# Optimization experiments

Hardware: AMD Instinct MI355X
Metric: run time of the kernel (lower is better)

The kernel has to match this reference:

```python
import jax, jax.numpy as jnp
import numpy as np

BS, IN_F, OUT_F = 1024, 128, 100000
M, S, ALPHA = 0.35, 30.0, 0.5


def _l2norm(x):
    # F.normalize: x / max(||x||, eps)
    n = jnp.sqrt(jnp.sum(x * x, axis=-1, keepdims=True))
    return x / jnp.maximum(n, 1e-12)


def setup_inputs() -> dict:
    key = jax.random.key(0)
    k1, k2, k3 = jax.random.split(key, 3)
    return {
        "input": jax.random.normal(k1, (BS, IN_F), dtype=jnp.float32),
        "label": jax.random.randint(k2, (BS,), 0, OUT_F, dtype=jnp.int64),
        "weight": jax.random.normal(k3, (OUT_F, IN_F), dtype=jnp.float32),
    }


def reference(input, label, weight):
    wn = _l2norm(weight)                      # [nc, d]
    fn = _l2norm(input)                       # [bs, d]
    logits = jnp.einsum('bd,cd->bc', fn, wn)  # [bs, nc] cosine sims
    bs = fn.shape[0]
    rows = jnp.arange(bs)

    pos = jnp.take_along_axis(logits, label[:, None], axis=1)[:, 0] * S  # [bs]
    # negatives: all classes except the label (replaces masked_select + view)
    neg = (logits * S).at[rows, label].set(-jnp.inf)
    lse_neg = jax.nn.logsumexp(neg, axis=1)   # [bs]

    # loss = mean(log(1 + exp(m + lse_neg - pos)))
    loss = jnp.mean(jax.nn.softplus(M + lse_neg - pos))

    # weight.data update: per-class mean of normalized features for classes
    # present in the batch (the torch loop is exactly a segment-mean; note
    # weight_update aliases weight.data so the final blend is a no-op and the
    # result is simply: present rows <- class mean, other rows unchanged).
    sums = jax.ops.segment_sum(fn, label, num_segments=OUT_F)                # [nc, d]
    counts = jax.ops.segment_sum(jnp.ones((bs,), fn.dtype), label, num_segments=OUT_F)
    present = counts > 0
    class_mean = sums / jnp.maximum(counts, 1.0)[:, None]
    new_weight = jnp.where(present[:, None], class_mean, weight)

    return loss, new_weight
```

## Files before the change

kernel.cpp:

```cpp
#include <hip/hip_runtime.h>

#define BS 1024
#define D 128
#define NC 100000
#define NCP 100096
#define NTILES 782
#define S_SCALE 30.0f
#define MARGIN 0.35f
#define GRIDX 64

typedef __attribute__((ext_vector_type(8))) short bf16x8;
typedef __attribute__((ext_vector_type(4))) float f32x4;

__device__ __forceinline__ unsigned short f2bf(float f) {
    union { float f; unsigned u; } x; x.f = f;
    unsigned u = x.u;
    u += 0x7FFFu + ((u >> 16) & 1u);
    return (unsigned short)(u >> 16);
}

__device__ __forceinline__ void gld_lds16(const void* g, void* l) {
    auto gp = (const __attribute__((address_space(1))) unsigned int*)(g);
    auto lp = (__attribute__((address_space(3))) unsigned int*)(l);
    __builtin_amdgcn_global_load_lds(gp, lp, 16, 0, 0);
}

__global__ void prep_fn(const float* __restrict__ inp, const int* __restrict__ label,
                        const float* __restrict__ wt,
                        float* __restrict__ fn_f32, unsigned short* __restrict__ fn_sw,
                        float* __restrict__ counts, float* __restrict__ pos) {
    int row = blockIdx.x;
    int lane = threadIdx.x;
    float2 v = *(const float2*)(inp + row * D + lane * 2);
    float s = v.x * v.x + v.y * v.y;
    #pragma unroll
    for (int m = 1; m < 64; m <<= 1) s += __shfl_xor(s, m);
    float inv = 1.0f / fmaxf(sqrtf(s), 1e-12f);
    float a = v.x * inv, b = v.y * inv;
    *(float2*)(fn_f32 + row * D + lane * 2) = make_float2(a, b);
    unsigned pack = (unsigned)f2bf(a) | ((unsigned)f2bf(b) << 16);
    ((unsigned*)fn_sw)[row * 64 + (((lane >> 2) ^ (row & 15)) << 2) + (lane & 3)] = pack;

    int c = label[row];
    float2 wv = *(const float2*)(wt + c * D + lane * 2);
    float sw_ = wv.x * wv.x + wv.y * wv.y;
    float dt  = wv.x * a + wv.y * b;
    #pragma unroll
    for (int m = 1; m < 64; m <<= 1) { sw_ += __shfl_xor(sw_, m); dt += __shfl_xor(dt, m); }
    if (lane == 0) {
        float invw = 1.0f / fmaxf(sqrtf(sw_), 1e-12f);
        pos[row] = S_SCALE * dt * invw;
        atomicAdd(counts + c, 1.0f);
    }
}

__global__ void prep_wn(const float* __restrict__ wt, const float* __restrict__ counts,
                        unsigned short* __restrict__ wn_sw, float* __restrict__ outw) {
    int wv = threadIdx.x >> 6, lane = threadIdx.x & 63;
    int row = blockIdx.x * 4 + wv;
    int t = row >> 7, c = row & 127;
    unsigned* dst = (unsigned*)wn_sw + t * 8192 + c * 64 +
                    (((lane >> 2) ^ (c & 15)) << 2) + (lane & 3);
    if (row < NC) {
        float2 v = *(const float2*)(wt + row * D + lane * 2);
        float s = v.x * v.x + v.y * v.y;
        #pragma unroll
        for (int m = 1; m < 64; m <<= 1) s += __shfl_xor(s, m);
        float inv = 1.0f / fmaxf(sqrtf(s), 1e-12f);
        *dst = (unsigned)f2bf(v.x * inv) | ((unsigned)f2bf(v.y * inv) << 16);
        float cnt = counts[row];
        float2 o = (cnt > 0.0f) ? make_float2(0.0f, 0.0f) : v;
        *(float2*)(outw + row * D + lane * 2) = o;
    } else {
        *dst = 0u;
    }
}

__global__ __launch_bounds__(256, 2) void main_gemm(
    const unsigned short* __restrict__ fnsw, const unsigned short* __restrict__ wnsw,
    float* __restrict__ sumexp) {
    __shared__ __align__(16) short As[128 * 128];
    __shared__ __align__(16) short Bs[128 * 128];
    int tid = threadIdx.x;
    int lane = tid & 63, w = tid >> 6;
    int quad = lane >> 4, l15 = lane & 15;
    int m0 = (w >> 1) * 64, n0 = (w & 1) * 64;
    int rowbase = blockIdx.y * 128;

    {
        const char* gA = (const char*)fnsw + rowbase * 256 + w * 8192 + lane * 16;
        char* lA = (char*)As + w * 8192;
        #pragma unroll
        for (int j = 0; j < 8; j++) gld_lds16(gA + j * 1024, lA + j * 1024);
    }

    float sums[16];
    #pragma unroll
    for (int i = 0; i < 16; i++) sums[i] = 0.0f;

    for (int tile = blockIdx.x; tile < NTILES; tile += GRIDX) {
        const char* gB = (const char*)wnsw + tile * 32768 + w * 8192 + lane * 16;
        char* lB = (char*)Bs + w * 8192;
        __syncthreads();
        #pragma unroll
        for (int j = 0; j < 8; j++) gld_lds16(gB + j * 1024, lB + j * 1024);
        __syncthreads();

        f32x4 acc[4][4];
        #pragma unroll
        for (int mt = 0; mt < 4; mt++)
            #pragma unroll
            for (int nt = 0; nt < 4; nt++)
                acc[mt][nt] = (f32x4){0.0f, 0.0f, 0.0f, 0.0f};

        #pragma unroll
        for (int ks = 0; ks < 4; ks++) {
            int kb = ks * 4 + quad;
            bf16x8 af[4], bf[4];
            #pragma unroll
            for (int mt = 0; mt < 4; mt++) {
                int row = m0 + mt * 16 + l15;
                af[mt] = *(const bf16x8*)(As + (row * 16 + (kb ^ l15)) * 8);
            }
            #pragma unroll
            for (int nt = 0; nt < 4; nt++) {
                int row = n0 + nt * 16 + l15;
                bf[nt] = *(const bf16x8*)(Bs + (row * 16 + (kb ^ l15)) * 8);
            }
            #pragma unroll
            for (int mt = 0; mt < 4; mt++)
                #pragma unroll
                for (int nt = 0; nt < 4; nt++)
                    acc[mt][nt] = __builtin_amdgcn_mfma_f32_16x16x32_bf16(
                        af[mt], bf[nt], acc[mt][nt], 0, 0, 0);
        }

        #pragma unroll
        for (int nt = 0; nt < 4; nt++)
            #pragma unroll
            for (int mt = 0; mt < 4; mt++)
                #pragma unroll
                for (int r = 0; r < 4; r++)
                    sums[mt * 4 + r] += __expf(fmaf(acc[mt][nt][r], S_SCALE, -30.0f));
    }

    #pragma unroll
    for (int mt = 0; mt < 4; mt++) {
        #pragma unroll
        for (int r = 0; r < 4; r++) {
            float s = sums[mt * 4 + r];
            s += __shfl_xor(s, 1);
            s += __shfl_xor(s, 2);
            s += __shfl_xor(s, 4);
            s += __shfl_xor(s, 8);
            if (l15 == 0)
                atomicAdd(sumexp + rowbase + m0 + mt * 16 + quad * 4 + r, s);
        }
    }
}

__global__ void loss_k(const float* __restrict__ sumexp, const float* __restrict__ pos,
                       float* __restrict__ out) {
    __shared__ float red[256];
    int t = threadIdx.x;
    float acc = 0.0f;
    #pragma unroll
    for (int i = 0; i < 4; i++) {
        int r = t + i * 256;
        float p = pos[r];
        float sneg = fmaxf(sumexp[r] - __expf(p - 30.0f), 1e-38f);
        float lse = 30.0f + logf(sneg);
        float z = MARGIN + lse - p;
        acc += fmaxf(z, 0.0f) + log1pf(__expf(-fabsf(z)));
    }
    red[t] = acc;
    __syncthreads();
    for (int s = 128; s > 0; s >>= 1) {
        if (t < s) red[t] += red[t + s];
        __syncthreads();
    }
    if (t == 0) out[0] = red[0] * (1.0f / 1024.0f);
}

__global__ void addmean_k(const float* __restrict__ fn_f32, const int* __restrict__ label,
                          const float* __restrict__ counts, float* __restrict__ outw) {
    int b = blockIdx.x, t = threadIdx.x;
    int c = label[b];
    float cnt = counts[c];
    atomicAdd(outw + c * D + t, fn_f32[b * D + t] / cnt);
}

extern "C" void kernel_launch(void* const* d_in, const int* in_sizes, int n_in,
                              void* d_out, int out_size, void* d_ws, size_t ws_size,
                              hipStream_t stream) {
    (void)in_sizes; (void)n_in; (void)out_size; (void)ws_size;
    const float* inp   = (const float*)d_in[0];
    const int*   label = (const int*)d_in[1];
    const float* wt    = (const float*)d_in[2];
    float* out = (float*)d_out;

    char* w = (char*)d_ws;
    float*          fn_f32 = (float*)(w);
    unsigned short* fn_sw  = (unsigned short*)(w + 524288);
    unsigned short* wn_sw  = (unsigned short*)(w + 786432);
    float*          sumexp = (float*)(w + 26411008);
    float*          counts = (float*)(w + 26415104);
    float*          pos    = (float*)(w + 26815104);

    hipMemsetAsync(w + 26411008, 0, 404096, stream);

    prep_fn<<<BS, 64, 0, stream>>>(inp, label, wt, fn_f32, fn_sw, counts, pos);
    prep_wn<<<NCP / 4, 256, 0, stream>>>(wt, counts, wn_sw, out + 1);
    main_gemm<<<dim3(GRIDX, 8), 256, 0, stream>>>(fn_sw, wn_sw, sumexp);
    addmean_k<<<BS, D, 0, stream>>>(fn_f32, label, counts, out + 1);
    loss_k<<<1, 256, 0, stream>>>(sumexp, pos, out);
}
```

Measured before the change: 162.7 us.

## Fuse loss and class-mean into prep/GEMM kernels, keep A in registers, use exp2

Several changes land together. The class-mean weight update moves into prep_fn, which accumulates per-slot sums, and prep_wn, which writes the mean directly, so the addmean kernel goes away. The loss reduction moves into the GEMM's last-finishing block through a ticket counter, so loss_k goes away. The GEMM now keeps the A fragments in registers with a single LDS buffer, folds the scale into the features so it can use exp2, and changes grid and occupancy (GRIDX 96, launch bounds 3). These cut launches and LDS traffic, at the cost of more atomics and higher register pressure.

```diff
diff --git a/kernel.cpp b/kernel.cpp
--- a/kernel.cpp
+++ b/kernel.cpp
@@ -7,7 +7,9 @@
 #define NTILES 782
 #define S_SCALE 30.0f
 #define MARGIN 0.35f
-#define GRIDX 64
+#define GRIDX 96
+#define GRID_TOTAL (GRIDX * 8)
+#define C_EXP 43.280851226668917f
 
 typedef __attribute__((ext_vector_type(8))) short bf16x8;
 typedef __attribute__((ext_vector_type(4))) float f32x4;
@@ -19,6 +21,14 @@
     return (unsigned short)(u >> 16);
 }
 
+__device__ __forceinline__ float fast_exp2(float x) {
+#if __has_builtin(__builtin_amdgcn_exp2f)
+    return __builtin_amdgcn_exp2f(x);
+#else
+    return exp2f(x);
+#endif
+}
+
 __device__ __forceinline__ void gld_lds16(const void* g, void* l) {
     auto gp = (const __attribute__((address_space(1))) unsigned int*)(g);
     auto lp = (__attribute__((address_space(3))) unsigned int*)(l);
@@ -27,34 +37,43 @@
 
 __global__ void prep_fn(const float* __restrict__ inp, const int* __restrict__ label,
                         const float* __restrict__ wt,
-                        float* __restrict__ fn_f32, unsigned short* __restrict__ fn_sw,
-                        float* __restrict__ counts, float* __restrict__ pos) {
-    int row = blockIdx.x;
-    int lane = threadIdx.x;
-    float2 v = *(const float2*)(inp + row * D + lane * 2);
+                        unsigned short* __restrict__ fn_sw,
+                        float* __restrict__ counts, int* __restrict__ class2slot,
+                        float* __restrict__ acc, float* __restrict__ pos) {
+    int wv = threadIdx.x >> 6, lane = threadIdx.x & 63;
+    int row = blockIdx.x * 4 + wv;
+    int c = label[row];
+    float2 v  = *(const float2*)(inp + row * D + lane * 2);
+    float2 wv2 = *(const float2*)(wt + c * D + lane * 2);
+
     float s = v.x * v.x + v.y * v.y;
     #pragma unroll
     for (int m = 1; m < 64; m <<= 1) s += __shfl_xor(s, m);
     float inv = 1.0f / fmaxf(sqrtf(s), 1e-12f);
     float a = v.x * inv, b = v.y * inv;
-    *(float2*)(fn_f32 + row * D + lane * 2) = make_float2(a, b);
-    unsigned pack = (unsigned)f2bf(a) | ((unsigned)f2bf(b) << 16);
+
+    unsigned pack = (unsigned)f2bf(a * C_EXP) | ((unsigned)f2bf(b * C_EXP) << 16);
     ((unsigned*)fn_sw)[row * 64 + (((lane >> 2) ^ (row & 15)) << 2) + (lane & 3)] = pack;
 
-    int c = label[row];
-    float2 wv = *(const float2*)(wt + c * D + lane * 2);
-    float sw_ = wv.x * wv.x + wv.y * wv.y;
-    float dt  = wv.x * a + wv.y * b;
+    float sw_ = wv2.x * wv2.x + wv2.y * wv2.y;
+    float dt  = wv2.x * a + wv2.y * b;
     #pragma unroll
     for (int m = 1; m < 64; m <<= 1) { sw_ += __shfl_xor(sw_, m); dt += __shfl_xor(dt, m); }
+
+    int slotrow = 0;
     if (lane == 0) {
-        float invw = 1.0f / fmaxf(sqrtf(sw_), 1e-12f);
-        pos[row] = S_SCALE * dt * invw;
+        pos[row] = S_SCALE * dt * (1.0f / fmaxf(sqrtf(sw_), 1e-12f));
         atomicAdd(counts + c, 1.0f);
-    }
+        int prev = atomicCAS(class2slot + c, 0, row + 1);
+        slotrow = prev ? (prev - 1) : row;
+    }
+    slotrow = __shfl(slotrow, 0);
+    atomicAdd(acc + slotrow * D + lane * 2,     a);
+    atomicAdd(acc + slotrow * D + lane * 2 + 1, b);
 }
 
 __global__ void prep_wn(const float* __restrict__ wt, const float* __restrict__ counts,
+                        const int* __restrict__ class2slot, const float* __restrict__ acc,
                         unsigned short* __restrict__ wn_sw, float* __restrict__ outw) {
     int wv = threadIdx.x >> 6, lane = threadIdx.x & 63;
     int row = blockIdx.x * 4 + wv;
@@ -69,18 +88,26 @@
         float inv = 1.0f / fmaxf(sqrtf(s), 1e-12f);
         *dst = (unsigned)f2bf(v.x * inv) | ((unsigned)f2bf(v.y * inv) << 16);
         float cnt = counts[row];
-        float2 o = (cnt > 0.0f) ? make_float2(0.0f, 0.0f) : v;
+        float2 o;
+        if (cnt > 0.0f) {
+            int sr = class2slot[row] - 1;
+            float rc = 1.0f / cnt;
+            o = make_float2(acc[sr * D + lane * 2] * rc, acc[sr * D + lane * 2 + 1] * rc);
+        } else {
+            o = v;
+        }
         *(float2*)(outw + row * D + lane * 2) = o;
     } else {
         *dst = 0u;
     }
 }
 
-__global__ __launch_bounds__(256, 2) void main_gemm(
+__global__ __launch_bounds__(256, 3) void main_gemm(
     const unsigned short* __restrict__ fnsw, const unsigned short* __restrict__ wnsw,
-    float* __restrict__ sumexp) {
-    __shared__ __align__(16) short As[128 * 128];
+    const float* __restrict__ pos, float* __restrict__ sumexp,
+    unsigned int* __restrict__ done, float* __restrict__ out) {
     __shared__ __align__(16) short Bs[128 * 128];
+    __shared__ unsigned int sticket;
     int tid = threadIdx.x;
     int lane = tid & 63, w = tid >> 6;
     int quad = lane >> 4, l15 = lane & 15;
@@ -89,59 +116,54 @@
 
     {
         const char* gA = (const char*)fnsw + rowbase * 256 + w * 8192 + lane * 16;
-        char* lA = (char*)As + w * 8192;
+        char* lA = (char*)Bs + w * 8192;
         #pragma unroll
         for (int j = 0; j < 8; j++) gld_lds16(gA + j * 1024, lA + j * 1024);
     }
+    __syncthreads();
+    bf16x8 af[4][4];
+    #pragma unroll
+    for (int mt = 0; mt < 4; mt++) {
+        int row = m0 + mt * 16 + l15;
+        #pragma unroll
+        for (int ks = 0; ks < 4; ks++)
+            af[mt][ks] = *(const bf16x8*)(Bs + (row * 16 + (((ks * 4 + quad)) ^ l15)) * 8);
+    }
 
     float sums[16];
     #pragma unroll
     for (int i = 0; i < 16; i++) sums[i] = 0.0f;
 
     for (int tile = blockIdx.x; tile < NTILES; tile += GRIDX) {
+        __syncthreads();
         const char* gB = (const char*)wnsw + tile * 32768 + w * 8192 + lane * 16;
         char* lB = (char*)Bs + w * 8192;
-        __syncthreads();
         #pragma unroll
         for (int j = 0; j < 8; j++) gld_lds16(gB + j * 1024, lB + j * 1024);
         __syncthreads();
 
-        f32x4 acc[4][4];
-        #pragma unroll
-        for (int mt = 0; mt < 4; mt++)
-            #pragma unroll
-            for (int nt = 0; nt < 4; nt++)
-                acc[mt][nt] = (f32x4){0.0f, 0.0f, 0.0f, 0.0f};
-
-        #pragma unroll
-        for (int ks = 0; ks < 4; ks++) {
-            int kb = ks * 4 + quad;
-            bf16x8 af[4], bf[4];
-            #pragma unroll
-            for (int mt = 0; mt < 4; mt++) {
-                int row = m0 + mt * 16 + l15;
-                af[mt] = *(const bf16x8*)(As + (row * 16 + (kb ^ l15)) * 8);
-            }
-            #pragma unroll
-            for (int nt = 0; nt < 4; nt++) {
-                int row = n0 + nt * 16 + l15;
-                bf[nt] = *(const bf16x8*)(Bs + (row * 16 + (kb ^ l15)) * 8);
-            }
-            #pragma unroll
-            for (int mt = 0; mt < 4; mt++)
+        #pragma unroll
+        for (int nt = 0; nt < 4; nt++) {
+            bf16x8 bf[4];
+            int brow = n0 + nt * 16 + l15;
+            #pragma unroll
+            for (int ks = 0; ks < 4; ks++)
+                bf[ks] = *(const bf16x8*)(Bs + (brow * 16 + ((ks * 4 + quad) ^ l15)) * 8);
+            f32x4 acc[4];
+            #pragma unroll
+            for (int mt = 0; mt < 4; mt++) acc[mt] = (f32x4){0.f, 0.f, 0.f, 0.f};
+            #pragma unroll
+            for (int ks = 0; ks < 4; ks++)
                 #pragma unroll
-                for (int nt = 0; nt < 4; nt++)
-                    acc[mt][nt] = __builtin_amdgcn_mfma_f32_16x16x32_bf16(
-                        af[mt], bf[nt], acc[mt][nt], 0, 0, 0);
-        }
-
-        #pragma unroll
-        for (int nt = 0; nt < 4; nt++)
+                for (int mt = 0; mt < 4; mt++)
+                    acc[mt] = __builtin_amdgcn_mfma_f32_16x16x32_bf16(
+                        af[mt][ks], bf[ks], acc[mt], 0, 0, 0);
             #pragma unroll
             for (int mt = 0; mt < 4; mt++)
                 #pragma unroll
                 for (int r = 0; r < 4; r++)
-                    sums[mt * 4 + r] += __expf(fmaf(acc[mt][nt][r], S_SCALE, -30.0f));
+                    sums[mt * 4 + r] += fast_exp2(acc[mt][r] - C_EXP);
+        }
     }
 
     #pragma unroll
@@ -157,37 +179,30 @@
                 atomicAdd(sumexp + rowbase + m0 + mt * 16 + quad * 4 + r, s);
         }
     }
-}
-
-__global__ void loss_k(const float* __restrict__ sumexp, const float* __restrict__ pos,
-                       float* __restrict__ out) {
-    __shared__ float red[256];
-    int t = threadIdx.x;
-    float acc = 0.0f;
-    #pragma unroll
-    for (int i = 0; i < 4; i++) {
-        int r = t + i * 256;
-        float p = pos[r];
-        float sneg = fmaxf(sumexp[r] - __expf(p - 30.0f), 1e-38f);
-        float lse = 30.0f + logf(sneg);
-        float z = MARGIN + lse - p;
-        acc += fmaxf(z, 0.0f) + log1pf(__expf(-fabsf(z)));
-    }
-    red[t] = acc;
+
+    __threadfence();
+    if (tid == 0) sticket = atomicAdd(done, 1u);
     __syncthreads();
-    for (int s = 128; s > 0; s >>= 1) {
-        if (t < s) red[t] += red[t + s];
+    if (sticket == GRID_TOTAL - 1) {
+        __shared__ float red[256];
+        float accv = 0.0f;
+        #pragma unroll
+        for (int i = 0; i < 4; i++) {
+            int r = tid + i * 256;
+            float se = atomicAdd(&sumexp[r], 0.0f);
+            float p = pos[r];
+            float sneg = fmaxf(se - __expf(p - 30.0f), 1e-38f);
+            float z = MARGIN + 30.0f + logf(sneg) - p;
+            accv += fmaxf(z, 0.0f) + log1pf(__expf(-fabsf(z)));
+        }
+        red[tid] = accv;
         __syncthreads();
-    }
-    if (t == 0) out[0] = red[0] * (1.0f / 1024.0f);
-}
-
-__global__ void addmean_k(const float* __restrict__ fn_f32, const int* __restrict__ label,
-                          const float* __restrict__ counts, float* __restrict__ outw) {
-    int b = blockIdx.x, t = threadIdx.x;
-    int c = label[b];
-    float cnt = counts[c];
-    atomicAdd(outw + c * D + t, fn_f32[b * D + t] / cnt);
+        for (int s = 128; s > 0; s >>= 1) {
+            if (tid < s) red[tid] += red[tid + s];
+            __syncthreads();
+        }
+        if (tid == 0) out[0] = red[0] * (1.0f / 1024.0f);
+    }
 }
 
 extern "C" void kernel_launch(void* const* d_in, const int* in_sizes, int n_in,
@@ -200,18 +215,18 @@
     float* out = (float*)d_out;
 
     char* w = (char*)d_ws;
-    float*          fn_f32 = (float*)(w);
-    unsigned short* fn_sw  = (unsigned short*)(w + 524288);
-    unsigned short* wn_sw  = (unsigned short*)(w + 786432);
-    float*          sumexp = (float*)(w + 26411008);
-    float*          counts = (float*)(w + 26415104);
-    float*          pos    = (float*)(w + 26815104);
-
-    hipMemsetAsync(w + 26411008, 0, 404096, stream);
-
-    prep_fn<<<BS, 64, 0, stream>>>(inp, label, wt, fn_f32, fn_sw, counts, pos);
-    prep_wn<<<NCP / 4, 256, 0, stream>>>(wt, counts, wn_sw, out + 1);
-    main_gemm<<<dim3(GRIDX, 8), 256, 0, stream>>>(fn_sw, wn_sw, sumexp);
-    addmean_k<<<BS, D, 0, stream>>>(fn_f32, label, counts, out + 1);
-    loss_k<<<1, 256, 0, stream>>>(sumexp, pos, out);
-}
+    unsigned short* fn_sw  = (unsigned short*)(w);
+    unsigned short* wn_sw  = (unsigned short*)(w + 262144);
+    float*        sumexp     = (float*)(w + 25886720);
+    float*        counts     = (float*)(w + 25890816);
+    int*          class2slot = (int*)  (w + 26291200);
+    float*        acc        = (float*)(w + 26691584);
+    unsigned int* done       = (unsigned int*)(w + 27215872);
+    float*        pos        = (float*)(w + 27216128);
+
+    hipMemsetAsync(w + 25886720, 0, 1329408, stream);
+
+    prep_fn<<<BS / 4, 256, 0, stream>>>(inp, label, wt, fn_sw, counts, class2slot, acc, pos);
+    prep_wn<<<NCP / 4, 256, 0, stream>>>(wt, counts, class2slot, acc, wn_sw, out + 1);
+    main_gemm<<<dim3(GRIDX, 8), 256, 0, stream>>>(fn_sw, wn_sw, pos, sumexp, done, out);
+}
```

Result: slower. 207.2 us (+27.4%).
